# Optimization experiments

Hardware: AMD Instinct MI355X
Metric: run time of the kernel (lower is better)

## Reference

```python
import jax, jax.numpy as jnp
import numpy as np

E, B, S, D, R = 8, 8, 2048, 512, 128
MAX_MAG = 0.1  # config.geometric.max_rotation_magnitude


def _plane_indices(dim, r):
    # Row-major enumeration of (i, j), i < j, truncated to first r planes,
    # matching the nested loop in create_rotation_matrix.
    pairs = []
    for i in range(dim):
        for j in range(i + 1, dim):
            pairs.append((i, j))
            if len(pairs) == r:
                return np.asarray(pairs, np.int32)
    return np.asarray(pairs, np.int32)


def setup_inputs() -> dict:
    key = jax.random.key(0)
    k1, k2, k3 = jax.random.split(key, 3)
    x = jax.random.normal(k1, (B, S, D), dtype=jnp.float32)
    theta = jax.random.normal(k2, (E, R), dtype=jnp.float32) * 0.1
    # projector init: 0.1 * orthogonal + I  (per torch init in __init__)
    Wr = jax.random.normal(k3, (E, D, D), dtype=jnp.float32)
    Q, _ = jnp.linalg.qr(Wr)
    proj_w = 0.1 * Q + jnp.eye(D, dtype=jnp.float32)
    return {"x": x, "theta": theta, "proj_w": proj_w}


def _rotation_matrix(theta_e, ij):
    # Sequential right-multiplication by Givens rotations.
    # M <- M @ G(i,j,a) only touches columns i and j:
    #   col_i' =  c*col_i + s*col_j ;  col_j' = -s*col_i + c*col_j
    angles = jnp.tanh(theta_e) * MAX_MAG  # [R]

    def step(M, inp):
        i, j, a = inp
        c, s = jnp.cos(a), jnp.sin(a)
        ci = M[:, i]
        cj = M[:, j]
        M = M.at[:, i].set(c * ci + s * cj)
        M = M.at[:, j].set(-s * ci + c * cj)
        return M, None

    M0 = jnp.eye(D, dtype=theta_e.dtype)
    M, _ = jax.lax.scan(step, M0, (ij[:, 0], ij[:, 1], angles))
    return M


def reference(x, theta, proj_w):
    ij = jnp.asarray(_plane_indices(D, R))  # [R, 2] static plane indices
    Rm = jax.vmap(lambda t: _rotation_matrix(t, ij))(theta)  # [E, D, D]
    # rotated = flat_x @ R^T per expert
    rotated = jnp.einsum('bsd,ekd->ebsk', x, Rm)            # [E, B, S, D]
    # projector: Linear(bias=False) -> y = rotated @ W^T
    out = jnp.einsum('ebsk,eok->ebso', rotated, proj_w)     # [E, B, S, D]
    return out
```

## Files before the change

kernel.cpp:

```cpp
#include <hip/hip_runtime.h>
#include <hip/hip_bf16.h>

#define E_ 8
#define B_ 8
#define S_ 2048
#define D_ 512
#define R_ 128
#define M_TOT (B_ * S_)

typedef __attribute__((ext_vector_type(8))) short bf16x8;
typedef __attribute__((ext_vector_type(4))) float f32x4;
typedef __attribute__((ext_vector_type(4))) short s16x4;

__device__ __forceinline__ void gload_lds16(void* lds, const void* g) {
  __builtin_amdgcn_global_load_lds(
      (const __attribute__((address_space(1))) void*)g,
      (__attribute__((address_space(3))) void*)lds, 16, 0, 0);
}

#define ROT_B 32
#define WT_B 2048
#define CX_B 4096
__global__ __launch_bounds__(256) void prep_fused(
    const float* __restrict__ x, const float* __restrict__ theta,
    const float* __restrict__ pw, __hip_bfloat16* __restrict__ xb,
    __hip_bfloat16* __restrict__ Wb) {
  int blk = blockIdx.x;
  int t = threadIdx.x;
  if (blk < ROT_B) {
    __shared__ float cs[R_], ss[R_];
    __shared__ float Pch[128][130];
    __shared__ __hip_bfloat16 Wch[128][130];
    int e = blk >> 2;
    int r0 = (blk & 3) * 128;
    if (t < R_) {
      float a = tanhf(theta[e * R_ + t]) * 0.1f;
      cs[t] = cosf(a);
      ss[t] = sinf(a);
    }
    const float* Pe = pw + (size_t)e * D_ * D_;
    __hip_bfloat16* We = Wb + (size_t)e * D_ * D_;
#pragma unroll 8
    for (int it = 0; it < 64; ++it) {
      int row = it * 2 + (t >> 7);
      int col = t & 127;
      Pch[row][col] = Pe[(size_t)(r0 + row) * D_ + col];
    }
    if (t < 128) Pch[t][128] = Pe[(size_t)(r0 + t) * D_ + 128];
    __syncthreads();
    if (t < 128) {
      float u = Pch[t][0];
#pragma unroll 16
      for (int k = 0; k < R_; ++k) {
        float pj = Pch[t][k + 1];
        Wch[t][k + 1] = __float2bfloat16(cs[k] * pj - ss[k] * u);
        u = cs[k] * u + ss[k] * pj;
      }
      Wch[t][0] = __float2bfloat16(u);
    }
    __syncthreads();
#pragma unroll 8
    for (int it = 0; it < 64; ++it) {
      int row = it * 2 + (t >> 7);
      int col = t & 127;
      We[(size_t)(r0 + row) * D_ + col] = Wch[row][col];
    }
    if (t < 128) We[(size_t)(r0 + t) * D_ + 128] = Wch[t][128];
  } else if (blk < ROT_B + WT_B) {
    int g = (blk - ROT_B) * 256 + t;
    int gidx = g & 127;
    if (gidx < 32) return;
    float4 v = ((const float4*)pw)[g];
    union { short4 s; __hip_bfloat16 h[4]; } u;
    u.h[0] = __float2bfloat16(v.x);
    u.h[1] = __float2bfloat16(v.y);
    u.h[2] = __float2bfloat16(v.z);
    u.h[3] = __float2bfloat16(v.w);
    if (gidx > 32) {
      ((short4*)Wb)[g] = u.s;
    } else {
      Wb[(size_t)g * 4 + 1] = u.h[1];
      Wb[(size_t)g * 4 + 2] = u.h[2];
      Wb[(size_t)g * 4 + 3] = u.h[3];
    }
  } else {
    int i = (blk - ROT_B - WT_B) * 256 + t;
#pragma unroll
    for (int rep = 0; rep < 2; ++rep) {
      int idx = i + rep * (CX_B * 256);
      f32x4 v = __builtin_nontemporal_load(&((const f32x4*)x)[idx]);
      union { s16x4 s; __hip_bfloat16 h[4]; } u;
      u.h[0] = __float2bfloat16(v.x);
      u.h[1] = __float2bfloat16(v.y);
      u.h[2] = __float2bfloat16(v.z);
      u.h[3] = __float2bfloat16(v.w);
      ((s16x4*)xb)[idx] = u.s;
    }
  }
}

__global__ __launch_bounds__(256, 2) void gemm_xw(
    const __hip_bfloat16* __restrict__ Xb,
    const __hip_bfloat16* __restrict__ Wb,
    float* __restrict__ out)
{
  constexpr int BM = 256, BN = 128, BK = 32;
  constexpr int KD = D_, ND = D_;
  constexpr int NT = KD / BK;
  __shared__ __align__(16) char smem[49152];
  __hip_bfloat16 (*As)[BM * BK] =
      (__hip_bfloat16 (*)[BM * BK]) & smem[0];
  __hip_bfloat16 (*Bs)[BN * BK] =
      (__hip_bfloat16 (*)[BN * BK]) & smem[32768];
  float* Lep = (float*)&smem[0];

  int bx = blockIdx.x;
  int xcd = bx & 7, c = bx >> 3;
  int e = c >> 5;
  int msub = (c >> 2) & 7;
  int nt = c & 3;
  int mt = xcd * 8 + msub;

  int tid = threadIdx.x;
  int wave = tid >> 6, lane = tid & 63;
  int lr = lane & 15, lk = lane >> 4;
  int wm = wave >> 1, wn = wave & 1;

  const __hip_bfloat16* Ag = Xb + (size_t)(mt * BM) * KD;
  const __hip_bfloat16* Bg = Wb + ((size_t)e * ND + (size_t)nt * BN) * KD;

  int srow = lane >> 2;
  int scol = (lane & 3) * 8;

  int aoff = (wm * 128 + lr) * BK + lk * 8;
  int boff = (wn * 64 + lr) * BK + lk * 8;

  f32x4 acc[8][4];
#pragma unroll
  for (int i = 0; i < 8; ++i)
#pragma unroll
    for (int j = 0; j < 4; ++j) acc[i][j] = (f32x4){0.f, 0.f, 0.f, 0.f};

#define STAGE(buf, t)                                                        \
  {                                                                          \
    _Pragma("unroll") for (int g = 0; g < 4; ++g) {                          \
      int rb = wave * 64 + g * 16;                                           \
      gload_lds16(&As[buf][rb * BK],                                         \
                  Ag + (size_t)(rb + srow) * KD + (t) * BK + scol);          \
    }                                                                        \
    _Pragma("unroll") for (int g = 0; g < 2; ++g) {                          \
      int rb = wave * 32 + g * 16;                                           \
      gload_lds16(&Bs[buf][rb * BK],                                         \
                  Bg + (size_t)(rb + srow) * KD + (t) * BK + scol);          \
    }                                                                        \
  }

  STAGE(0, 0);
  STAGE(1, 1);

#pragma unroll
  for (int t = 0; t < NT; ++t) {
    int buf = t & 1;
    if (t < NT - 1) {
      asm volatile("s_waitcnt vmcnt(6)" ::: "memory");
    } else {
      asm volatile("s_waitcnt vmcnt(0)" ::: "memory");
    }
    __builtin_amdgcn_s_barrier();

    bf16x8 af[8], bfr[4];
#pragma unroll
    for (int ni = 0; ni < 4; ++ni)
      bfr[ni] = *(const bf16x8*)&Bs[buf][boff + ni * 16 * BK];
#pragma unroll
    for (int mi = 0; mi < 8; ++mi)
      af[mi] = *(const bf16x8*)&As[buf][aoff + mi * 16 * BK];
    __builtin_amdgcn_s_setprio(1);
#pragma unroll
    for (int mi = 0; mi < 8; ++mi)
#pragma unroll
      for (int ni = 0; ni < 4; ++ni)
        acc[mi][ni] = __builtin_amdgcn_mfma_f32_16x16x32_bf16(
            bfr[ni], af[mi], acc[mi][ni], 0, 0, 0);
    __builtin_amdgcn_s_setprio(0);

    asm volatile("s_waitcnt lgkmcnt(0)" ::: "memory");
    __builtin_amdgcn_sched_barrier(0);
    __builtin_amdgcn_s_barrier();
    if (t + 2 < NT) STAGE(buf, t + 2);
  }
#undef STAGE

  size_t obase = (size_t)e * M_TOT * ND;
  int row0 = mt * BM;
  int col0 = nt * BN;
  float* Lh = Lep + (size_t)wm * (32 * 132);
#pragma unroll
  for (int r = 0; r < 4; ++r) {
#pragma unroll
    for (int m2 = 0; m2 < 2; ++m2) {
      int mi = 2 * r + m2;
#pragma unroll
      for (int ni = 0; ni < 4; ++ni)
        *(f32x4*)&Lh[(m2 * 16 + lr) * 132 + wn * 64 + ni * 16 + lk * 4] =
            acc[mi][ni];
    }
    __builtin_amdgcn_s_barrier();
#pragma unroll
    for (int j = 0; j < 8; ++j) {
      int lrow = wn * 16 + j * 2 + (lane >> 5);
      int lc4 = lane & 31;
      f32x4 v = *(const f32x4*)&Lh[lrow * 132 + lc4 * 4];
      int grow = row0 + wm * 128 + r * 32 + lrow;
      __builtin_nontemporal_store(
          v, (f32x4*)&out[obase + (size_t)grow * ND + col0 + lc4 * 4]);
    }
    __builtin_amdgcn_s_barrier();
  }
}

extern "C" void kernel_launch(void* const* d_in, const int* in_sizes, int n_in,
                              void* d_out, int out_size, void* d_ws, size_t ws_size,
                              hipStream_t stream) {
  const float* x = (const float*)d_in[0];
  const float* theta = (const float*)d_in[1];
  const float* proj_w = (const float*)d_in[2];
  float* out = (float*)d_out;

  __hip_bfloat16* xb = (__hip_bfloat16*)d_ws;
  __hip_bfloat16* Wb = (__hip_bfloat16*)((char*)d_ws +
                        (size_t)M_TOT * D_ * sizeof(__hip_bfloat16));

  hipLaunchKernelGGL(prep_fused, dim3(ROT_B + WT_B + CX_B), dim3(256), 0,
                     stream, x, theta, proj_w, xb, Wb);
  hipLaunchKernelGGL(gemm_xw, dim3(2048), dim3(256), 0, stream, xb, Wb, out);
}
```

Before: 103.8 us.

## Fuse fp32-to-bf16 conversion of x into GEMM A-tile staging

Removes the separate pass that converted x to bf16 in workspace; the GEMM now loads fp32 x tiles into registers, converts them, and writes bf16 into LDS. This eliminates a full read and write of x through HBM and one portion of the prep kernel. In exchange, A-tile loads can no longer use direct global-to-LDS transfers, each block reads twice the bytes for A, and the register round-trip exposes load latency inside the main loop.

```diff
diff --git a/kernel.cpp b/kernel.cpp
--- a/kernel.cpp
+++ b/kernel.cpp
@@ -20,10 +20,8 @@
 
 #define ROT_B 32
 #define WT_B 2048
-#define CX_B 4096
-__global__ __launch_bounds__(256) void prep_fused(
-    const float* __restrict__ x, const float* __restrict__ theta,
-    const float* __restrict__ pw, __hip_bfloat16* __restrict__ xb,
+__global__ __launch_bounds__(256) void prep_w(
+    const float* __restrict__ theta, const float* __restrict__ pw,
     __hip_bfloat16* __restrict__ Wb) {
   int blk = blockIdx.x;
   int t = threadIdx.x;
@@ -66,7 +64,7 @@
       We[(size_t)(r0 + row) * D_ + col] = Wch[row][col];
     }
     if (t < 128) We[(size_t)(r0 + t) * D_ + 128] = Wch[t][128];
-  } else if (blk < ROT_B + WT_B) {
+  } else {
     int g = (blk - ROT_B) * 256 + t;
     int gidx = g & 127;
     if (gidx < 32) return;
@@ -83,24 +81,11 @@
       Wb[(size_t)g * 4 + 2] = u.h[2];
       Wb[(size_t)g * 4 + 3] = u.h[3];
     }
-  } else {
-    int i = (blk - ROT_B - WT_B) * 256 + t;
-#pragma unroll
-    for (int rep = 0; rep < 2; ++rep) {
-      int idx = i + rep * (CX_B * 256);
-      f32x4 v = __builtin_nontemporal_load(&((const f32x4*)x)[idx]);
-      union { s16x4 s; __hip_bfloat16 h[4]; } u;
-      u.h[0] = __float2bfloat16(v.x);
-      u.h[1] = __float2bfloat16(v.y);
-      u.h[2] = __float2bfloat16(v.z);
-      u.h[3] = __float2bfloat16(v.w);
-      ((s16x4*)xb)[idx] = u.s;
-    }
   }
 }
 
 __global__ __launch_bounds__(256, 2) void gemm_xw(
-    const __hip_bfloat16* __restrict__ Xb,
+    const float* __restrict__ Xf,
     const __hip_bfloat16* __restrict__ Wb,
     float* __restrict__ out)
 {
@@ -126,11 +111,13 @@
   int lr = lane & 15, lk = lane >> 4;
   int wm = wave >> 1, wn = wave & 1;
 
-  const __hip_bfloat16* Ag = Xb + (size_t)(mt * BM) * KD;
+  const float* Ag = Xf + (size_t)(mt * BM) * KD;
   const __hip_bfloat16* Bg = Wb + ((size_t)e * ND + (size_t)nt * BN) * KD;
 
   int srow = lane >> 2;
   int scol = (lane & 3) * 8;
+  int arow = lane >> 3;
+  int acol = (lane & 7) * 4;
 
   int aoff = (wm * 128 + lr) * BK + lk * 8;
   int boff = (wn * 64 + lr) * BK + lk * 8;
@@ -141,13 +128,25 @@
 #pragma unroll
     for (int j = 0; j < 4; ++j) acc[i][j] = (f32x4){0.f, 0.f, 0.f, 0.f};
 
-#define STAGE(buf, t)                                                        \
+#define ASTAGE(buf, t)                                                       \
   {                                                                          \
-    _Pragma("unroll") for (int g = 0; g < 4; ++g) {                          \
-      int rb = wave * 64 + g * 16;                                           \
-      gload_lds16(&As[buf][rb * BK],                                         \
-                  Ag + (size_t)(rb + srow) * KD + (t) * BK + scol);          \
+    f32x4 ar[8];                                                             \
+    _Pragma("unroll") for (int j = 0; j < 8; ++j) {                          \
+      int row = wave * 64 + j * 8 + arow;                                    \
+      ar[j] = *(const f32x4*)(Ag + (size_t)row * KD + (t) * BK + acol);      \
     }                                                                        \
+    _Pragma("unroll") for (int j = 0; j < 8; ++j) {                          \
+      int row = wave * 64 + j * 8 + arow;                                    \
+      union { s16x4 s; __hip_bfloat16 h[4]; } u;                             \
+      u.h[0] = __float2bfloat16(ar[j].x);                                    \
+      u.h[1] = __float2bfloat16(ar[j].y);                                    \
+      u.h[2] = __float2bfloat16(ar[j].z);                                    \
+      u.h[3] = __float2bfloat16(ar[j].w);                                    \
+      *(s16x4*)&As[buf][row * BK + acol] = u.s;                              \
+    }                                                                        \
+  }
+#define BLOAD(buf, t)                                                        \
+  {                                                                          \
     _Pragma("unroll") for (int g = 0; g < 2; ++g) {                          \
       int rb = wave * 32 + g * 16;                                           \
       gload_lds16(&Bs[buf][rb * BK],                                         \
@@ -155,17 +154,20 @@
     }                                                                        \
   }
 
-  STAGE(0, 0);
-  STAGE(1, 1);
+  BLOAD(0, 0); BLOAD(1, 1);
+  ASTAGE(0, 0);
+  ASTAGE(1, 1);
 
 #pragma unroll
   for (int t = 0; t < NT; ++t) {
     int buf = t & 1;
     if (t < NT - 1) {
-      asm volatile("s_waitcnt vmcnt(6)" ::: "memory");
+      asm volatile("s_waitcnt vmcnt(2)" ::: "memory");
     } else {
       asm volatile("s_waitcnt vmcnt(0)" ::: "memory");
     }
+    asm volatile("s_waitcnt lgkmcnt(0)" ::: "memory");
+    __builtin_amdgcn_sched_barrier(0);
     __builtin_amdgcn_s_barrier();
 
     bf16x8 af[8], bfr[4];
@@ -187,9 +189,13 @@
     asm volatile("s_waitcnt lgkmcnt(0)" ::: "memory");
     __builtin_amdgcn_sched_barrier(0);
     __builtin_amdgcn_s_barrier();
-    if (t + 2 < NT) STAGE(buf, t + 2);
-  }
-#undef STAGE
+    if (t + 2 < NT) {
+      BLOAD(buf, t + 2);
+      ASTAGE(buf, t + 2);
+    }
+  }
+#undef ASTAGE
+#undef BLOAD
 
   size_t obase = (size_t)e * M_TOT * ND;
   int row0 = mt * BM;
@@ -227,11 +233,9 @@
   const float* proj_w = (const float*)d_in[2];
   float* out = (float*)d_out;
 
-  __hip_bfloat16* xb = (__hip_bfloat16*)d_ws;
-  __hip_bfloat16* Wb = (__hip_bfloat16*)((char*)d_ws +
-                        (size_t)M_TOT * D_ * sizeof(__hip_bfloat16));
-
-  hipLaunchKernelGGL(prep_fused, dim3(ROT_B + WT_B + CX_B), dim3(256), 0,
-                     stream, x, theta, proj_w, xb, Wb);
-  hipLaunchKernelGGL(gemm_xw, dim3(2048), dim3(256), 0, stream, xb, Wb, out);
-}
+  __hip_bfloat16* Wb = (__hip_bfloat16*)d_ws;
+
+  hipLaunchKernelGGL(prep_w, dim3(ROT_B + WT_B), dim3(256), 0,
+                     stream, theta, proj_w, Wb);
+  hipLaunchKernelGGL(gemm_xw, dim3(2048), dim3(256), 0, stream, x, Wb, out);
+}
```

Measured after the change: 125.1 us. 20.5% more time.
